# Optimization experiments

Measured on AMD Instinct MI355X. Metric: run time of the kernel, lower is better.

Reference implementation:

```python
import jax, jax.numpy as jnp
import numpy as np
from math import atanh

B, T, D_IN, H = 16, 1024, 512, 1024
INIT_A = atanh(0.95)


def setup_inputs() -> dict:
    key = jax.random.key(0)
    k1, k2, k3, k4 = jax.random.split(key, 4)
    x = jax.random.normal(k1, (B, T, D_IN), dtype=jnp.float32)
    h0 = jax.random.normal(k2, (B, H), dtype=jnp.float32)
    # raw_a initialized near atanh(0.95) as in the module, with small jitter
    raw_a = INIT_A + 0.01 * jax.random.normal(k3, (H,), dtype=jnp.float32)
    # xavier-uniform for W_x.weight [H, D_IN]
    limit = float(np.sqrt(6.0 / (D_IN + H)))
    W = jax.random.uniform(k4, (H, D_IN), dtype=jnp.float32, minval=-limit, maxval=limit)
    b = jnp.zeros((H,), dtype=jnp.float32)
    return {"x": x, "h0": h0, "raw_a": raw_a, "W": W, "b": b}


def reference(x, h0, raw_a, W, b):
    # h_t = a * h_{t-1} + W x_t + b, computed via cumprod/cumsum parallel-scan trick
    a = jnp.tanh(raw_a)                                   # [H] (rho is None)
    z = jnp.einsum('btd,hd->bth', x, W) + b               # [B,T,H]
    A = jnp.broadcast_to(a, (x.shape[1], a.shape[0]))     # [T,H]
    p = jnp.cumprod(A, axis=0)[None]                      # [1,T,H], p[t] = a^(t+1)
    v = jnp.cumsum(z / jnp.maximum(p, 1e-12), axis=1)     # [B,T,H]
    h = v * p + p * h0[:, None, :]                        # include initial state
    zero_mask = (jnp.abs(a) < 1e-6)[None, None, :]        # degenerate a ~ 0 channels
    h = jnp.where(zero_mask, z, h)
    return h
```

## Files before the change

### kernel.cpp

```cpp
#include <hip/hip_runtime.h>
#include <cstdint>

#define B_DIM 16
#define T_DIM 1024
#define DK    512
#define H_DIM 1024

#define TCH    128
#define NCH    (T_DIM / TCH)
#define NB     64
#define NSTRIP (H_DIM / NB)
#define NKT    16
#define BKQ    4

typedef __bf16 bf16x8 __attribute__((ext_vector_type(8)));
typedef __bf16 bf16x4 __attribute__((ext_vector_type(4)));
typedef float  f32x4  __attribute__((ext_vector_type(4)));

typedef __attribute__((address_space(1))) unsigned int* as1p;
typedef __attribute__((address_space(3))) unsigned int* as3p;

__device__ __forceinline__ void async_cp16(const void* g, void* l) {
  __builtin_amdgcn_global_load_lds((as1p)(uint64_t)g,
                                   (as3p)(uint32_t)(uint64_t)l, 16, 0, 0);
}

__global__ __launch_bounds__(256) void prep(const float* __restrict__ x,
                                            __bf16* __restrict__ xbt,
                                            const float* __restrict__ W,
                                            __bf16* __restrict__ wbT,
                                            const float* __restrict__ raw_a,
                                            float4* __restrict__ meta,
                                            unsigned long long* __restrict__ flags) {
  const int bid = blockIdx.x, tid = threadIdx.x;
  if (bid < 4096) {
    const int g = bid * 256 + tid;
    const int b = g >> 16;
    const int r = g & 65535;
    const int kq = ((r >> 12) << 2) | (tid & 3);
    const int t  = (((r >> 6) & 63) << 4) | ((tid & 63) >> 2);
    const float* src = x + ((size_t)(b * T_DIM + t) * DK + kq * 8);
    f32x4 v0 = ((const f32x4*)src)[0];
    f32x4 v1 = ((const f32x4*)src)[1];
    bf16x8 o;
    o[0] = (__bf16)v0.x; o[1] = (__bf16)v0.y; o[2] = (__bf16)v0.z; o[3] = (__bf16)v0.w;
    o[4] = (__bf16)v1.x; o[5] = (__bf16)v1.y; o[6] = (__bf16)v1.z; o[7] = (__bf16)v1.w;
    *(bf16x8*)(xbt + ((size_t)(b * 64 + kq) * T_DIM + t) * 8) = o;
  } else if (bid < 4608) {
    const int i = (bid - 4096) * 256 + tid;
    const int h  = i >> 7;
    const int k0 = (i & 127) * 4;
    f32x4 v = ((const f32x4*)W)[i];
    bf16x4 o;
    o.x = (__bf16)v.x; o.y = (__bf16)v.y; o.z = (__bf16)v.z; o.w = (__bf16)v.w;
    *(bf16x4*)(wbT + ((size_t)(k0 >> 3) * H_DIM + h) * 8 + (k0 & 7)) = o;
  } else if (bid < 4612) {
    const int h = (bid - 4608) * 256 + tid;
    const float a = tanhf(raw_a[h]);
    const float la2 = log2f(fabsf(a));
    meta[h] = make_float4(a, la2, (a < 0.f) ? 1.f : 0.f, (fabsf(a) < 1e-6f) ? 1.f : 0.f);
  } else {
    flags[(bid - 4612) * 256 + tid] = 0ULL;
  }
}

__global__ __launch_bounds__(256, 4) void fused_rnn(
    const __bf16* __restrict__ xbt,
    const __bf16* __restrict__ wbT,
    const float* __restrict__ bias,
    const float4* __restrict__ meta,
    const float* __restrict__ h0g,
    unsigned long long* __restrict__ flags,
    float* __restrict__ out) {
  __shared__ __align__(16) __bf16 As[3][BKQ][TCH][8];
  __shared__ __align__(16) __bf16 Bs[3][BKQ][NB][8];
  __shared__ float chunkTot[2][NB];
  __shared__ float colCarry[NB];

  const int tid  = threadIdx.x;
  const int wave = tid >> 6;
  const int lane = tid & 63;
  const int q  = lane >> 4;
  const int c  = lane & 15;
  const int rw = wave & 1;
  const int cg = wave >> 1;

  const int bid   = blockIdx.x;
  const int g     = bid & 127;
  const int strip = bid >> 7;
  const int b     = g >> 3;
  const int chunk = g & 7;
  const int t0    = chunk * TCH;
  const int n0    = strip * NB;

  float bias_j[2], la2_j[2], h0_j[2];
  bool neg_j[2], zm_j[2];
#pragma unroll
  for (int j = 0; j < 2; ++j) {
    const int col = n0 + cg * 32 + j * 16 + c;
    bias_j[j] = bias[col];
    const float4 mt = meta[col];
    la2_j[j] = mt.y;
    neg_j[j] = mt.z != 0.f;
    zm_j[j]  = mt.w != 0.f;
    h0_j[j]  = h0g[(size_t)b * H_DIM + col];
  }

  auto stage = [&](int kt, int buf) {
    const int kq0 = kt * BKQ;
#pragma unroll
    for (int it = 0; it < 2; ++it) {
      const int s = it * 256 + tid;
      const int kq = s >> 7, row = s & 127;
      async_cp16(xbt + ((size_t)(b * 64 + kq0 + kq) * T_DIM + t0 + row) * 8,
                 &As[buf][kq][row][0]);
    }
    {
      const int kq = tid >> 6, col = tid & 63;
      async_cp16(wbT + ((size_t)(kq0 + kq) * H_DIM + n0 + col) * 8,
                 &Bs[buf][kq][col][0]);
    }
  };

  f32x4 acc[4][2];
#pragma unroll
  for (int i = 0; i < 4; ++i)
#pragma unroll
    for (int j = 0; j < 2; ++j) acc[i][j] = (f32x4){0.f, 0.f, 0.f, 0.f};

  stage(0, 0); stage(1, 1); stage(2, 2);

  int buf = 0;
  for (int kt = 0; kt < NKT; ++kt) {
    if (kt < NKT - 2)       asm volatile("s_waitcnt vmcnt(6)" ::: "memory");
    else if (kt == NKT - 2) asm volatile("s_waitcnt vmcnt(3)" ::: "memory");
    else                    asm volatile("s_waitcnt vmcnt(0)" ::: "memory");
    __builtin_amdgcn_s_barrier();
    bf16x8 af[4], bfr[2];
#pragma unroll
    for (int i = 0; i < 4; ++i)
      af[i] = *(const bf16x8*)(&As[buf][q][rw * 64 + i * 16 + c][0]);
#pragma unroll
    for (int j = 0; j < 2; ++j)
      bfr[j] = *(const bf16x8*)(&Bs[buf][q][cg * 32 + j * 16 + c][0]);
#pragma unroll
    for (int i = 0; i < 4; ++i)
#pragma unroll
      for (int j = 0; j < 2; ++j)
        acc[i][j] = __builtin_amdgcn_mfma_f32_16x16x32_bf16(af[i], bfr[j], acc[i][j], 0, 0, 0);
    __builtin_amdgcn_sched_barrier(0);
    __builtin_amdgcn_s_barrier();
    if (kt < NKT - 3) stage(kt + 3, buf);
    buf = (buf == 2) ? 0 : buf + 1;
  }

  f32x4 vloc[4][2];
  float icarry[2] = {0.f, 0.f};
#pragma unroll
  for (int i = 0; i < 4; ++i) {
#pragma unroll
    for (int j = 0; j < 2; ++j) {
      const float la2 = la2_j[j];
      f32x4 w;
#pragma unroll
      for (int r = 0; r < 4; ++r) {
        const int tp1 = t0 + rw * 64 + i * 16 + q * 4 + r + 1;
        const float z = acc[i][j][r] + bias_j[j];
        float inv = fminf(__builtin_amdgcn_exp2f(-la2 * (float)tp1), 1e12f);
        if (neg_j[j] && (tp1 & 1)) inv = 1e12f;
        w[r] = z * inv;
      }
      const float pr0 = w[0];
      const float pr1 = pr0 + w[1];
      const float pr2 = pr1 + w[2];
      const float pr3 = pr2 + w[3];
      const float x1 = __shfl_xor(pr3, 16, 64);
      const float x2 = __shfl_xor(pr3, 32, 64);
      const float x3 = __shfl_xor(pr3, 48, 64);
      float sq = 0.f;
      if (q >= 2) sq += x2 + x3;
      if (q & 1) sq += x1;
      const float base = icarry[j] + sq;
      vloc[i][j] = (f32x4){base + pr0, base + pr1, base + pr2, base + pr3};
      icarry[j] += pr3 + x1 + x2 + x3;
    }
  }
  if (q == 0) {
#pragma unroll
    for (int j = 0; j < 2; ++j) chunkTot[rw][cg * 32 + j * 16 + c] = icarry[j];
  }
  __syncthreads();

  if (tid < NB) {
    const int col = tid;
    const size_t fb = ((size_t)b * NSTRIP + strip) * NCH * NB;
    const float tot = chunkTot[0][col] + chunkTot[1][col];
    atomicExch(&flags[fb + (size_t)chunk * NB + col],
               (1ULL << 32) | (unsigned long long)__float_as_uint(tot));
    float s = 0.f;
    for (int p = 0; p < chunk; ++p) {
      unsigned long long v = atomicAdd(&flags[fb + (size_t)p * NB + col], 0ULL);
      while (!(v >> 32)) {
        __builtin_amdgcn_s_sleep(4);
        v = atomicAdd(&flags[fb + (size_t)p * NB + col], 0ULL);
      }
      s += __uint_as_float((unsigned int)v);
    }
    colCarry[col] = s;
  }
  __syncthreads();

  float cc[2];
#pragma unroll
  for (int j = 0; j < 2; ++j) {
    const int colL = cg * 32 + j * 16 + c;
    float s = colCarry[colL];
    if (rw) s += chunkTot[0][colL];
    cc[j] = s;
  }
#pragma unroll
  for (int i = 0; i < 4; ++i) {
#pragma unroll
    for (int j = 0; j < 2; ++j) {
      const float la2 = la2_j[j];
      const int col = n0 + cg * 32 + j * 16 + c;
#pragma unroll
      for (int r = 0; r < 4; ++r) {
        const int tl = t0 + rw * 64 + i * 16 + q * 4 + r;
        const int tp1 = tl + 1;
        float pv = __builtin_amdgcn_exp2f(la2 * (float)tp1);
        if (neg_j[j] && (tp1 & 1)) pv = -pv;
        const float v = cc[j] + vloc[i][j][r];
        const float hv = pv * v + pv * h0_j[j];
        const float zval = acc[i][j][r] + bias_j[j];
        out[(size_t)(b * T_DIM + tl) * H_DIM + col] = zm_j[j] ? zval : hv;
      }
    }
  }
}

extern "C" void kernel_launch(void* const* d_in, const int* in_sizes, int n_in,
                              void* d_out, int out_size, void* d_ws, size_t ws_size,
                              hipStream_t stream) {
  const float* x     = (const float*)d_in[0];
  const float* h0    = (const float*)d_in[1];
  const float* raw_a = (const float*)d_in[2];
  const float* W     = (const float*)d_in[3];
  const float* bias  = (const float*)d_in[4];
  float* out = (float*)d_out;

  char* ws = (char*)d_ws;
  __bf16* xbt = (__bf16*)(ws);
  __bf16* wbT = (__bf16*)(ws + 16777216);
  float4* meta = (float4*)(ws + 16777216 + 1048576);
  unsigned long long* flags =
      (unsigned long long*)(ws + 16777216 + 1048576 + 16384);

  prep<<<5124, 256, 0, stream>>>(x, xbt, W, wbT, raw_a, meta, flags);
  fused_rnn<<<2048, 256, 0, stream>>>(xbt, wbT, bias, meta, h0, flags, out);
}
```

Measured before the change: 135.2 us.

## Widen column strip to 128, fold bias into accumulator, use recurrent power products

Doubles the N-strip per block from 64 to 128 columns, so each wave computes a 4x4 MFMA tile, A-tile reuse rises, and the grid halves to 1024 blocks with the occupancy hint lowered to 3. Bias now initialises the accumulators. The per-element exp2 calls are replaced by one exp2 per group of four rows, followed by repeated multiplication by a or 1/a. The zero-a path recovers z from prefix differences. This trades fewer blocks and more registers per thread for less exp work and more data reuse, at some risk to precision and occupancy.

```diff
diff --git a/kernel.cpp b/kernel.cpp
--- a/kernel.cpp
+++ b/kernel.cpp
@@ -8,7 +8,7 @@
 
 #define TCH    128
 #define NCH    (T_DIM / TCH)
-#define NB     64
+#define NB     128
 #define NSTRIP (H_DIM / NB)
 #define NKT    16
 #define BKQ    4
@@ -64,7 +64,7 @@
   }
 }
 
-__global__ __launch_bounds__(256, 4) void fused_rnn(
+__global__ __launch_bounds__(256, 3) void fused_rnn(
     const __bf16* __restrict__ xbt,
     const __bf16* __restrict__ wbT,
     const float* __restrict__ bias,
@@ -93,15 +93,17 @@
   const int t0    = chunk * TCH;
   const int n0    = strip * NB;
 
-  float bias_j[2], la2_j[2], h0_j[2];
-  bool neg_j[2], zm_j[2];
-#pragma unroll
-  for (int j = 0; j < 2; ++j) {
-    const int col = n0 + cg * 32 + j * 16 + c;
+  float bias_j[4], la2_j[4], a_j[4], ai_j[4], sgn_j[4], h0_j[4];
+  bool zm_j[4];
+#pragma unroll
+  for (int j = 0; j < 4; ++j) {
+    const int col = n0 + cg * 64 + j * 16 + c;
     bias_j[j] = bias[col];
     const float4 mt = meta[col];
+    a_j[j]   = mt.x;
     la2_j[j] = mt.y;
-    neg_j[j] = mt.z != 0.f;
+    ai_j[j]  = 1.f / mt.x;
+    sgn_j[j] = (mt.z != 0.f) ? -1.f : 1.f;
     zm_j[j]  = mt.w != 0.f;
     h0_j[j]  = h0g[(size_t)b * H_DIM + col];
   }
@@ -115,38 +117,41 @@
       async_cp16(xbt + ((size_t)(b * 64 + kq0 + kq) * T_DIM + t0 + row) * 8,
                  &As[buf][kq][row][0]);
     }
-    {
-      const int kq = tid >> 6, col = tid & 63;
+#pragma unroll
+    for (int it = 0; it < 2; ++it) {
+      const int s = it * 256 + tid;
+      const int kq = s >> 7, col = s & 127;
       async_cp16(wbT + ((size_t)(kq0 + kq) * H_DIM + n0 + col) * 8,
                  &Bs[buf][kq][col][0]);
     }
   };
 
-  f32x4 acc[4][2];
+  f32x4 acc[4][4];
 #pragma unroll
   for (int i = 0; i < 4; ++i)
 #pragma unroll
-    for (int j = 0; j < 2; ++j) acc[i][j] = (f32x4){0.f, 0.f, 0.f, 0.f};
+    for (int j = 0; j < 4; ++j)
+      acc[i][j] = (f32x4){bias_j[j], bias_j[j], bias_j[j], bias_j[j]};
 
   stage(0, 0); stage(1, 1); stage(2, 2);
 
   int buf = 0;
   for (int kt = 0; kt < NKT; ++kt) {
-    if (kt < NKT - 2)       asm volatile("s_waitcnt vmcnt(6)" ::: "memory");
-    else if (kt == NKT - 2) asm volatile("s_waitcnt vmcnt(3)" ::: "memory");
+    if (kt < NKT - 2)       asm volatile("s_waitcnt vmcnt(8)" ::: "memory");
+    else if (kt == NKT - 2) asm volatile("s_waitcnt vmcnt(4)" ::: "memory");
     else                    asm volatile("s_waitcnt vmcnt(0)" ::: "memory");
     __builtin_amdgcn_s_barrier();
-    bf16x8 af[4], bfr[2];
+    bf16x8 af[4], bfr[4];
 #pragma unroll
     for (int i = 0; i < 4; ++i)
       af[i] = *(const bf16x8*)(&As[buf][q][rw * 64 + i * 16 + c][0]);
 #pragma unroll
-    for (int j = 0; j < 2; ++j)
-      bfr[j] = *(const bf16x8*)(&Bs[buf][q][cg * 32 + j * 16 + c][0]);
+    for (int j = 0; j < 4; ++j)
+      bfr[j] = *(const bf16x8*)(&Bs[buf][q][cg * 64 + j * 16 + c][0]);
 #pragma unroll
     for (int i = 0; i < 4; ++i)
 #pragma unroll
-      for (int j = 0; j < 2; ++j)
+      for (int j = 0; j < 4; ++j)
         acc[i][j] = __builtin_amdgcn_mfma_f32_16x16x32_bf16(af[i], bfr[j], acc[i][j], 0, 0, 0);
     __builtin_amdgcn_sched_barrier(0);
     __builtin_amdgcn_s_barrier();
@@ -154,26 +159,26 @@
     buf = (buf == 2) ? 0 : buf + 1;
   }
 
-  f32x4 vloc[4][2];
-  float icarry[2] = {0.f, 0.f};
+  float base_[4][4];
+  float icarry[4] = {0.f, 0.f, 0.f, 0.f};
 #pragma unroll
   for (int i = 0; i < 4; ++i) {
-#pragma unroll
-    for (int j = 0; j < 2; ++j) {
-      const float la2 = la2_j[j];
-      f32x4 w;
+    const int tp10 = t0 + rw * 64 + i * 16 + q * 4 + 1;
+#pragma unroll
+    for (int j = 0; j < 4; ++j) {
+      float u = __builtin_amdgcn_exp2f(-la2_j[j] * (float)tp10) * sgn_j[j];
+      f32x4 wv;
 #pragma unroll
       for (int r = 0; r < 4; ++r) {
-        const int tp1 = t0 + rw * 64 + i * 16 + q * 4 + r + 1;
-        const float z = acc[i][j][r] + bias_j[j];
-        float inv = fminf(__builtin_amdgcn_exp2f(-la2 * (float)tp1), 1e12f);
-        if (neg_j[j] && (tp1 & 1)) inv = 1e12f;
-        w[r] = z * inv;
+        const float uu = fminf(u, 1e12f);
+        const float inv = (u < 0.f) ? 1e12f : uu;
+        wv[r] = acc[i][j][r] * inv;
+        u *= ai_j[j];
       }
-      const float pr0 = w[0];
-      const float pr1 = pr0 + w[1];
-      const float pr2 = pr1 + w[2];
-      const float pr3 = pr2 + w[3];
+      const float pr0 = wv[0];
+      const float pr1 = pr0 + wv[1];
+      const float pr2 = pr1 + wv[2];
+      const float pr3 = pr2 + wv[3];
       const float x1 = __shfl_xor(pr3, 16, 64);
       const float x2 = __shfl_xor(pr3, 32, 64);
       const float x3 = __shfl_xor(pr3, 48, 64);
@@ -181,13 +186,14 @@
       if (q >= 2) sq += x2 + x3;
       if (q & 1) sq += x1;
       const float base = icarry[j] + sq;
-      vloc[i][j] = (f32x4){base + pr0, base + pr1, base + pr2, base + pr3};
+      base_[i][j] = base;
+      acc[i][j] = (f32x4){base + pr0, base + pr1, base + pr2, base + pr3};
       icarry[j] += pr3 + x1 + x2 + x3;
     }
   }
   if (q == 0) {
 #pragma unroll
-    for (int j = 0; j < 2; ++j) chunkTot[rw][cg * 32 + j * 16 + c] = icarry[j];
+    for (int j = 0; j < 4; ++j) chunkTot[rw][cg * 64 + j * 16 + c] = icarry[j];
   }
   __syncthreads();
 
@@ -210,30 +216,28 @@
   }
   __syncthreads();
 
-  float cc[2];
-#pragma unroll
-  for (int j = 0; j < 2; ++j) {
-    const int colL = cg * 32 + j * 16 + c;
+  float cc_[4];
+#pragma unroll
+  for (int j = 0; j < 4; ++j) {
+    const int colL = cg * 64 + j * 16 + c;
     float s = colCarry[colL];
     if (rw) s += chunkTot[0][colL];
-    cc[j] = s;
+    cc_[j] = s + h0_j[j];
   }
 #pragma unroll
   for (int i = 0; i < 4; ++i) {
-#pragma unroll
-    for (int j = 0; j < 2; ++j) {
-      const float la2 = la2_j[j];
-      const int col = n0 + cg * 32 + j * 16 + c;
+    const int tp10 = t0 + rw * 64 + i * 16 + q * 4 + 1;
+#pragma unroll
+    for (int j = 0; j < 4; ++j) {
+      float pv = __builtin_amdgcn_exp2f(la2_j[j] * (float)tp10) * sgn_j[j];
+      const int col = n0 + cg * 64 + j * 16 + c;
 #pragma unroll
       for (int r = 0; r < 4; ++r) {
         const int tl = t0 + rw * 64 + i * 16 + q * 4 + r;
-        const int tp1 = tl + 1;
-        float pv = __builtin_amdgcn_exp2f(la2 * (float)tp1);
-        if (neg_j[j] && (tp1 & 1)) pv = -pv;
-        const float v = cc[j] + vloc[i][j][r];
-        const float hv = pv * v + pv * h0_j[j];
-        const float zval = acc[i][j][r] + bias_j[j];
-        out[(size_t)(b * T_DIM + tl) * H_DIM + col] = zm_j[j] ? zval : hv;
+        const float hv = pv * (acc[i][j][r] + cc_[j]);
+        const float wr = acc[i][j][r] - ((r == 0) ? base_[i][j] : acc[i][j][r - 1]);
+        out[(size_t)(b * T_DIM + tl) * H_DIM + col] = zm_j[j] ? wr * 1e-12f : hv;
+        pv *= a_j[j];
       }
     }
   }
@@ -257,5 +261,5 @@
       (unsigned long long*)(ws + 16777216 + 1048576 + 16384);
 
   prep<<<5124, 256, 0, stream>>>(x, xbt, W, wbT, raw_a, meta, flags);
-  fused_rnn<<<2048, 256, 0, stream>>>(xbt, wbT, bias, meta, h0, flags, out);
-}
+  fused_rnn<<<1024, 256, 0, stream>>>(xbt, wbT, bias, meta, h0, flags, out);
+}
```

Measured after the change: 124.3 us. 1.09x faster.
